# Kernel optimization log

Hardware: AMD Instinct MI355X
Metric: run time of the kernel (lower is better)

## Reference

```python
import jax, jax.numpy as jnp
import numpy as np

B, T, S, H, L = 64, 512, 400, 768, 9


def setup_inputs() -> dict:
    rng = np.random.default_rng(0)
    attn = np.zeros((B, T), np.int32)
    ids_lens = np.zeros((B, S), np.int32)
    for bi in range(B):
        Lb = int(rng.integers(T // 2, T + 1))  # valid wordpiece count
        lens = []
        rem = Lb
        while rem > 0 and len(lens) < S - 1:
            l = int(min(rng.integers(1, 4), rem))  # 1-3 wordpieces per word
            lens.append(l)
            rem -= l
        if rem > 0:
            lens.append(rem)
        attn[bi, :Lb] = 1
        ids_lens[bi, :len(lens)] = np.asarray(lens, np.int32)
    label_ids = rng.integers(0, L, (B, S)).astype(np.int32)
    label_mask = ids_lens > 0
    key = jax.random.key(0)
    k1, k2 = jax.random.split(key)
    last_enc_out = jax.random.normal(k1, (B, T, H), jnp.float32)
    W = jax.random.normal(k2, (H, L), jnp.float32) * 0.02
    b = jnp.zeros((L,), jnp.float32)
    return {
        'last_enc_out': last_enc_out, 'W': W, 'b': b,
        'attention_mask': jnp.asarray(attn), 'ids_lens': jnp.asarray(ids_lens),
        'label_ids': jnp.asarray(label_ids), 'label_mask': jnp.asarray(label_mask),
    }


def reference(last_enc_out, W, b, attention_mask, ids_lens, label_ids, label_mask):
    Bv, Tv, Hv = last_enc_out.shape
    Sv = ids_lens.shape[1]
    # position of each valid token among the row's valid tokens
    tok_pos = jnp.cumsum(attention_mask, axis=1) - 1            # [B,T]
    cum = jnp.cumsum(ids_lens, axis=1)                          # [B,S] nondecreasing
    # word index for each token: first w with cum[w] > tok_pos
    word_idx = jax.vmap(lambda c, p: jnp.searchsorted(c, p, side='right'))(cum, tok_pos)
    valid = attention_mask > 0
    seg = jnp.where(valid, jnp.arange(Bv)[:, None] * Sv + word_idx, Bv * Sv)  # dump slot for pad
    sums = jax.ops.segment_sum(last_enc_out.reshape(Bv * Tv, Hv), seg.reshape(Bv * Tv),
                               num_segments=Bv * Sv + 1)[:Bv * Sv]
    counts = jnp.maximum(ids_lens.reshape(Bv * Sv), 1).astype(last_enc_out.dtype)
    means = (sums / counts[:, None]).reshape(Bv, Sv, Hv)
    word_mask = ids_lens > 0
    bert_embed = jnp.where(word_mask[:, :, None], means, jnp.zeros((), last_enc_out.dtype))
    # dropout is identity in eval mode
    logits = bert_embed @ W + b                                 # [B,S,L]
    logp = jax.nn.log_softmax(logits, axis=-1)
    nll = -jnp.take_along_axis(logp, label_ids[..., None].astype(jnp.int32), axis=-1)[..., 0]
    mf = label_mask.astype(logits.dtype)
    loss = jnp.sum(nll * mf) / jnp.sum(mf)                      # CE with ignore_index masking
    output = jnp.argmax(logits, axis=-1)
    return loss, output
```

## Files before the change

### kernel.cpp

```cpp
#include <hip/hip_runtime.h>
#include <math.h>

#define Bdim 64
#define Tdim 512
#define Sdim 400
#define Hdim 768
#define Ldim 9
#define PSTRIDE 12

#define PROJ_BLOCKS 2048
#define TOK_PER_BLK 16

template <int CTRL>
__device__ __forceinline__ float dpp_add(float x) {
  int y = __builtin_amdgcn_update_dpp(0, __float_as_int(x), CTRL, 0xF, 0xF, false);
  return x + __int_as_float(y);
}
__device__ __forceinline__ float wave_sum63(float x) {
  x = dpp_add<0x111>(x);
  x = dpp_add<0x112>(x);
  x = dpp_add<0x114>(x);
  x = dpp_add<0x118>(x);
  x = dpp_add<0x142>(x);
  x = dpp_add<0x143>(x);
  return x;
}

__global__ __launch_bounds__(Tdim) void setup_kernel(
    const int* __restrict__ attn, const int* __restrict__ ids_lens,
    int* __restrict__ pos2tok, int* __restrict__ wstart,
    int* __restrict__ nvalid, float* __restrict__ accum,
    unsigned* __restrict__ counter) {
  int b = blockIdx.x;
  int tid = threadIdx.x;
  int lane = tid & 63, wid = tid >> 6;
  __shared__ int wsum[8];
  __shared__ int totsm;

  if (b == 0 && tid < 2) accum[tid] = 0.0f;
  if (b == 0 && tid == 2) *counter = 0u;

  int m = attn[b * Tdim + tid];
  int x = m;
#pragma unroll
  for (int off = 1; off < 64; off <<= 1) {
    int v = __shfl_up(x, off, 64);
    if (lane >= off) x += v;
  }
  if (lane == 63) wsum[wid] = x;
  __syncthreads();
  if (tid < 8) {
    int s = wsum[tid];
    int y = s;
#pragma unroll
    for (int off = 1; off < 8; off <<= 1) {
      int v = __shfl_up(y, off, 64);
      if (tid >= off) y += v;
    }
    wsum[tid] = y - s;
    if (tid == 7) totsm = y;
  }
  __syncthreads();
  int total = totsm;
  x += wsum[wid];
  if (m) pos2tok[b * Tdim + x - 1] = tid;
  if (tid == 0) nvalid[b] = total;
  __syncthreads();

  int len = (tid < Sdim) ? ids_lens[b * Sdim + tid] : 0;
  int x2 = len;
#pragma unroll
  for (int off = 1; off < 64; off <<= 1) {
    int v = __shfl_up(x2, off, 64);
    if (lane >= off) x2 += v;
  }
  if (lane == 63) wsum[wid] = x2;
  __syncthreads();
  if (tid < 8) {
    int s = wsum[tid];
    int y = s;
#pragma unroll
    for (int off = 1; off < 8; off <<= 1) {
      int v = __shfl_up(y, off, 64);
      if (tid >= off) y += v;
    }
    wsum[tid] = y - s;
  }
  __syncthreads();
  x2 += wsum[wid];
  if (tid < Sdim) wstart[b * Sdim + tid] = x2 - len;
}

__global__ __launch_bounds__(192, 4) void proj_kernel(
    const float* __restrict__ enc, const float* __restrict__ W,
    const int* __restrict__ pos2tok, const int* __restrict__ nvalid,
    float* __restrict__ proj) {
  int tid = threadIdx.x;
  int lane = tid & 63;
  int w = tid >> 6;
  int l0 = w * 3;
  int base = blockIdx.x * TOK_PER_BLK;
  int b = base >> 9;
  int vc = nvalid[b] - (base & 511);
  vc = vc < 0 ? 0 : (vc > TOK_PER_BLK ? TOK_PER_BLK : vc);
  if (vc == 0) return;

  float wf[3][4][3];
#pragma unroll
  for (int k = 0; k < 3; ++k)
#pragma unroll
    for (int j = 0; j < 4; ++j) {
      int h = 4 * lane + 256 * k + j;
#pragma unroll
      for (int c = 0; c < 3; ++c) wf[k][j][c] = W[(size_t)h * Ldim + l0 + c];
    }

  const float4* encb = (const float4*)enc + (size_t)(b << 9) * (Hdim / 4);

  float4 xr[2][3];
#pragma unroll
  for (int i = 0; i < 2; ++i) {
    int tv = pos2tok[base + i];
    int t = (i < vc) ? tv : 0;
    const float4* r = encb + (size_t)t * (Hdim / 4);
    xr[i][0] = r[lane];
    xr[i][1] = r[lane + 64];
    xr[i][2] = r[lane + 128];
  }

#pragma unroll
  for (int i = 0; i < TOK_PER_BLK; ++i) {
    float4 x0 = xr[i & 1][0], x1 = xr[i & 1][1], x2 = xr[i & 1][2];
    if (i < vc) {
      float dd[3];
#pragma unroll
      for (int c = 0; c < 3; ++c) {
        dd[c] = x0.x * wf[0][0][c] + x0.y * wf[0][1][c] +
                x0.z * wf[0][2][c] + x0.w * wf[0][3][c] +
                x1.x * wf[1][0][c] + x1.y * wf[1][1][c] +
                x1.z * wf[1][2][c] + x1.w * wf[1][3][c] +
                x2.x * wf[2][0][c] + x2.y * wf[2][1][c] +
                x2.z * wf[2][2][c] + x2.w * wf[2][3][c];
      }
#pragma unroll
      for (int c = 0; c < 3; ++c) dd[c] = wave_sum63(dd[c]);
      if (lane == 63) {
        float* dst = proj + (size_t)(base + i) * PSTRIDE + l0;
        dst[0] = dd[0];
        dst[1] = dd[1];
        dst[2] = dd[2];
      }
    }
    if (i + 2 < TOK_PER_BLK) {
      int tv = pos2tok[base + i + 2];
      int t = (i + 2 < vc) ? tv : 0;
      const float4* r = encb + (size_t)t * (Hdim / 4);
      xr[i & 1][0] = r[lane];
      xr[i & 1][1] = r[lane + 64];
      xr[i & 1][2] = r[lane + 128];
    }
  }
}

__global__ __launch_bounds__(256) void word_kernel(
    const float* __restrict__ proj, const float* __restrict__ bias,
    const int* __restrict__ ids_lens, const int* __restrict__ label_ids,
    const int* __restrict__ wstart, const int* __restrict__ nvalid,
    float* __restrict__ out, float* __restrict__ accum,
    unsigned* __restrict__ counter) {
  int bs = blockIdx.x * 256 + threadIdx.x;
  int b = bs / Sdim;
  int len = ids_lens[bs];

  float s[Ldim];
#pragma unroll
  for (int l = 0; l < Ldim; ++l) s[l] = 0.0f;

  if (len > 0) {
    int start = wstart[bs];
    int nv = nvalid[b];
    for (int j = 0; j < len; ++j) {
      int q = start + j;
      if (q >= nv) break;
      const float* pr = proj + ((size_t)(b << 9) + q) * PSTRIDE;
#pragma unroll
      for (int l = 0; l < Ldim; ++l) s[l] += pr[l];
    }
  }
  float inv = (len > 0) ? 1.0f / (float)len : 0.0f;
  float lg[Ldim];
#pragma unroll
  for (int l = 0; l < Ldim; ++l) lg[l] = s[l] * inv + bias[l];

  int amax = 0;
  float mx = lg[0];
#pragma unroll
  for (int l = 1; l < Ldim; ++l)
    if (lg[l] > mx) { mx = lg[l]; amax = l; }
  out[1 + bs] = (float)amax;

  float nll = 0.0f, cnt = 0.0f;
  if (len > 0) {
    float se = 0.0f;
#pragma unroll
    for (int l = 0; l < Ldim; ++l) se += expf(lg[l] - mx);
    float lse = mx + logf(se);
    int lab = label_ids[bs];
    float ll = lg[0];
#pragma unroll
    for (int l = 1; l < Ldim; ++l) ll = (lab == l) ? lg[l] : ll;
    nll = lse - ll;
    cnt = 1.0f;
  }

#pragma unroll
  for (int off = 32; off > 0; off >>= 1) {
    nll += __shfl_down(nll, off, 64);
    cnt += __shfl_down(cnt, off, 64);
  }
  __shared__ float ss[4], cc[4];
  int wid = threadIdx.x >> 6, lane = threadIdx.x & 63;
  if (lane == 0) { ss[wid] = nll; cc[wid] = cnt; }
  __syncthreads();
  if (threadIdx.x == 0) {
    atomicAdd(&accum[0], ss[0] + ss[1] + ss[2] + ss[3]);
    atomicAdd(&accum[1], cc[0] + cc[1] + cc[2] + cc[3]);
    __threadfence();
    unsigned prev = atomicAdd(counter, 1u);
    if (prev == gridDim.x - 1) {
      __threadfence();
      float S = atomicAdd(&accum[0], 0.0f);
      float C = atomicAdd(&accum[1], 0.0f);
      out[0] = S / C;
    }
  }
}

extern "C" void kernel_launch(void* const* d_in, const int* in_sizes, int n_in,
                              void* d_out, int out_size, void* d_ws, size_t ws_size,
                              hipStream_t stream) {
  const float* enc      = (const float*)d_in[0];
  const float* W        = (const float*)d_in[1];
  const float* bias     = (const float*)d_in[2];
  const int* attn       = (const int*)d_in[3];
  const int* ids_lens   = (const int*)d_in[4];
  const int* label_ids  = (const int*)d_in[5];

  float* out = (float*)d_out;

  char* ws = (char*)d_ws;
  size_t off0 = 0;
  int* pos2tok      = (int*)(ws + off0);      off0 += (size_t)Bdim * Tdim * sizeof(int);
  int* wstart       = (int*)(ws + off0);      off0 += (size_t)Bdim * Sdim * sizeof(int);
  int* nvalid       = (int*)(ws + off0);      off0 += 256;
  float* accum      = (float*)(ws + off0);    off0 += 128;
  unsigned* counter = (unsigned*)(ws + off0); off0 += 128;
  float* proj       = (float*)(ws + off0);    off0 += (size_t)Bdim * Tdim * PSTRIDE * sizeof(float);

  int word_blocks = (Bdim * Sdim) / 256;

  setup_kernel<<<Bdim, Tdim, 0, stream>>>(attn, ids_lens, pos2tok, wstart,
                                          nvalid, accum, counter);
  proj_kernel<<<PROJ_BLOCKS, 192, 0, stream>>>(enc, W, pos2tok, nvalid, proj);
  word_kernel<<<word_blocks, 256, 0, stream>>>(proj, bias, ids_lens, label_ids,
                                               wstart, nvalid, out, accum, counter);
}
```

Baseline: 39.32 us.

## Fuse setup, projection and word stages into one cooperative kernel with grid syncs

```diff
diff --git a/kernel.cpp b/kernel.cpp
--- a/kernel.cpp
+++ b/kernel.cpp
@@ -1,5 +1,8 @@
 #include <hip/hip_runtime.h>
+#include <hip/hip_cooperative_groups.h>
 #include <math.h>
+
+namespace cg = cooperative_groups;
 
 #define Bdim 64
 #define Tdim 512
@@ -8,8 +11,10 @@
 #define Ldim 9
 #define PSTRIDE 12
 
-#define PROJ_BLOCKS 2048
-#define TOK_PER_BLK 16
+#define NBLK 256
+#define NTHR 256
+#define SLOTS 128
+#define WPB 100
 
 template <int CTRL>
 __device__ __forceinline__ float dpp_add(float x) {
@@ -26,242 +31,233 @@
   return x;
 }
 
-__global__ __launch_bounds__(Tdim) void setup_kernel(
-    const int* __restrict__ attn, const int* __restrict__ ids_lens,
+__global__ __launch_bounds__(NTHR, 1) void fused_kernel(
+    const float* __restrict__ enc, const float* __restrict__ W,
+    const float* __restrict__ bias, const int* __restrict__ attn,
+    const int* __restrict__ ids_lens, const int* __restrict__ label_ids,
     int* __restrict__ pos2tok, int* __restrict__ wstart,
-    int* __restrict__ nvalid, float* __restrict__ accum,
-    unsigned* __restrict__ counter) {
-  int b = blockIdx.x;
-  int tid = threadIdx.x;
-  int lane = tid & 63, wid = tid >> 6;
-  __shared__ int wsum[8];
-  __shared__ int totsm;
-
-  if (b == 0 && tid < 2) accum[tid] = 0.0f;
-  if (b == 0 && tid == 2) *counter = 0u;
-
-  int m = attn[b * Tdim + tid];
-  int x = m;
-#pragma unroll
-  for (int off = 1; off < 64; off <<= 1) {
-    int v = __shfl_up(x, off, 64);
-    if (lane >= off) x += v;
-  }
-  if (lane == 63) wsum[wid] = x;
-  __syncthreads();
-  if (tid < 8) {
-    int s = wsum[tid];
-    int y = s;
-#pragma unroll
-    for (int off = 1; off < 8; off <<= 1) {
-      int v = __shfl_up(y, off, 64);
-      if (tid >= off) y += v;
-    }
-    wsum[tid] = y - s;
-    if (tid == 7) totsm = y;
-  }
-  __syncthreads();
-  int total = totsm;
-  x += wsum[wid];
-  if (m) pos2tok[b * Tdim + x - 1] = tid;
-  if (tid == 0) nvalid[b] = total;
-  __syncthreads();
-
-  int len = (tid < Sdim) ? ids_lens[b * Sdim + tid] : 0;
-  int x2 = len;
-#pragma unroll
-  for (int off = 1; off < 64; off <<= 1) {
-    int v = __shfl_up(x2, off, 64);
-    if (lane >= off) x2 += v;
-  }
-  if (lane == 63) wsum[wid] = x2;
-  __syncthreads();
-  if (tid < 8) {
-    int s = wsum[tid];
-    int y = s;
-#pragma unroll
-    for (int off = 1; off < 8; off <<= 1) {
-      int v = __shfl_up(y, off, 64);
-      if (tid >= off) y += v;
-    }
-    wsum[tid] = y - s;
-  }
-  __syncthreads();
-  x2 += wsum[wid];
-  if (tid < Sdim) wstart[b * Sdim + tid] = x2 - len;
-}
-
-__global__ __launch_bounds__(192, 4) void proj_kernel(
-    const float* __restrict__ enc, const float* __restrict__ W,
-    const int* __restrict__ pos2tok, const int* __restrict__ nvalid,
-    float* __restrict__ proj) {
-  int tid = threadIdx.x;
-  int lane = tid & 63;
-  int w = tid >> 6;
-  int l0 = w * 3;
-  int base = blockIdx.x * TOK_PER_BLK;
-  int b = base >> 9;
-  int vc = nvalid[b] - (base & 511);
-  vc = vc < 0 ? 0 : (vc > TOK_PER_BLK ? TOK_PER_BLK : vc);
-  if (vc == 0) return;
-
-  float wf[3][4][3];
-#pragma unroll
-  for (int k = 0; k < 3; ++k)
-#pragma unroll
-    for (int j = 0; j < 4; ++j) {
-      int h = 4 * lane + 256 * k + j;
-#pragma unroll
-      for (int c = 0; c < 3; ++c) wf[k][j][c] = W[(size_t)h * Ldim + l0 + c];
-    }
-
-  const float4* encb = (const float4*)enc + (size_t)(b << 9) * (Hdim / 4);
-
-  float4 xr[2][3];
-#pragma unroll
-  for (int i = 0; i < 2; ++i) {
-    int tv = pos2tok[base + i];
-    int t = (i < vc) ? tv : 0;
-    const float4* r = encb + (size_t)t * (Hdim / 4);
-    xr[i][0] = r[lane];
-    xr[i][1] = r[lane + 64];
-    xr[i][2] = r[lane + 128];
-  }
-
-#pragma unroll
-  for (int i = 0; i < TOK_PER_BLK; ++i) {
-    float4 x0 = xr[i & 1][0], x1 = xr[i & 1][1], x2 = xr[i & 1][2];
-    if (i < vc) {
-      float dd[3];
-#pragma unroll
-      for (int c = 0; c < 3; ++c) {
-        dd[c] = x0.x * wf[0][0][c] + x0.y * wf[0][1][c] +
-                x0.z * wf[0][2][c] + x0.w * wf[0][3][c] +
-                x1.x * wf[1][0][c] + x1.y * wf[1][1][c] +
-                x1.z * wf[1][2][c] + x1.w * wf[1][3][c] +
-                x2.x * wf[2][0][c] + x2.y * wf[2][1][c] +
-                x2.z * wf[2][2][c] + x2.w * wf[2][3][c];
-      }
-#pragma unroll
-      for (int c = 0; c < 3; ++c) dd[c] = wave_sum63(dd[c]);
-      if (lane == 63) {
-        float* dst = proj + (size_t)(base + i) * PSTRIDE + l0;
-        dst[0] = dd[0];
-        dst[1] = dd[1];
-        dst[2] = dd[2];
-      }
-    }
-    if (i + 2 < TOK_PER_BLK) {
-      int tv = pos2tok[base + i + 2];
-      int t = (i + 2 < vc) ? tv : 0;
-      const float4* r = encb + (size_t)t * (Hdim / 4);
-      xr[i & 1][0] = r[lane];
-      xr[i & 1][1] = r[lane + 64];
-      xr[i & 1][2] = r[lane + 128];
-    }
-  }
-}
-
-__global__ __launch_bounds__(256) void word_kernel(
-    const float* __restrict__ proj, const float* __restrict__ bias,
-    const int* __restrict__ ids_lens, const int* __restrict__ label_ids,
-    const int* __restrict__ wstart, const int* __restrict__ nvalid,
-    float* __restrict__ out, float* __restrict__ accum,
-    unsigned* __restrict__ counter) {
-  int bs = blockIdx.x * 256 + threadIdx.x;
-  int b = bs / Sdim;
-  int len = ids_lens[bs];
-
-  float s[Ldim];
-#pragma unroll
-  for (int l = 0; l < Ldim; ++l) s[l] = 0.0f;
-
-  if (len > 0) {
-    int start = wstart[bs];
-    int nv = nvalid[b];
-    for (int j = 0; j < len; ++j) {
-      int q = start + j;
-      if (q >= nv) break;
-      const float* pr = proj + ((size_t)(b << 9) + q) * PSTRIDE;
-#pragma unroll
-      for (int l = 0; l < Ldim; ++l) s[l] += pr[l];
-    }
-  }
-  float inv = (len > 0) ? 1.0f / (float)len : 0.0f;
-  float lg[Ldim];
-#pragma unroll
-  for (int l = 0; l < Ldim; ++l) lg[l] = s[l] * inv + bias[l];
-
-  int amax = 0;
-  float mx = lg[0];
-#pragma unroll
-  for (int l = 1; l < Ldim; ++l)
-    if (lg[l] > mx) { mx = lg[l]; amax = l; }
-  out[1 + bs] = (float)amax;
-
-  float nll = 0.0f, cnt = 0.0f;
-  if (len > 0) {
-    float se = 0.0f;
-#pragma unroll
-    for (int l = 0; l < Ldim; ++l) se += expf(lg[l] - mx);
-    float lse = mx + logf(se);
-    int lab = label_ids[bs];
-    float ll = lg[0];
-#pragma unroll
-    for (int l = 1; l < Ldim; ++l) ll = (lab == l) ? lg[l] : ll;
-    nll = lse - ll;
-    cnt = 1.0f;
-  }
-
-#pragma unroll
-  for (int off = 32; off > 0; off >>= 1) {
-    nll += __shfl_down(nll, off, 64);
-    cnt += __shfl_down(cnt, off, 64);
-  }
-  __shared__ float ss[4], cc[4];
-  int wid = threadIdx.x >> 6, lane = threadIdx.x & 63;
-  if (lane == 0) { ss[wid] = nll; cc[wid] = cnt; }
-  __syncthreads();
-  if (threadIdx.x == 0) {
-    atomicAdd(&accum[0], ss[0] + ss[1] + ss[2] + ss[3]);
-    atomicAdd(&accum[1], cc[0] + cc[1] + cc[2] + cc[3]);
-    __threadfence();
-    unsigned prev = atomicAdd(counter, 1u);
-    if (prev == gridDim.x - 1) {
-      __threadfence();
-      float S = atomicAdd(&accum[0], 0.0f);
-      float C = atomicAdd(&accum[1], 0.0f);
-      out[0] = S / C;
-    }
+    int* __restrict__ nvalid, float* __restrict__ proj,
+    float2* __restrict__ partials, float* __restrict__ out) {
+  cg::grid_group grid = cg::this_grid();
+  int blk = blockIdx.x, tid = threadIdx.x;
+  int lane = tid & 63, w = tid >> 6;
+  __shared__ int wsum[4];
+  __shared__ int tot;
+  __shared__ float ssm[4], csm[4];
+
+  if (blk < Bdim) {
+    int b = blk;
+    int a0 = attn[b * Tdim + 2 * tid];
+    int a1 = attn[b * Tdim + 2 * tid + 1];
+    int pr = a0 + a1, x = pr;
+#pragma unroll
+    for (int off = 1; off < 64; off <<= 1) {
+      int v = __shfl_up(x, off, 64);
+      if (lane >= off) x += v;
+    }
+    if (lane == 63) wsum[w] = x;
+    __syncthreads();
+    if (tid < 4) {
+      int s = wsum[tid], y = s;
+#pragma unroll
+      for (int off = 1; off < 4; off <<= 1) {
+        int v = __shfl_up(y, off, 64);
+        if (tid >= off) y += v;
+      }
+      wsum[tid] = y - s;
+      if (tid == 3) tot = y;
+    }
+    __syncthreads();
+    int excl = x + wsum[w] - pr;
+    if (a0) pos2tok[b * Tdim + excl + a0 - 1] = 2 * tid;
+    if (a1) pos2tok[b * Tdim + excl + a0 + a1 - 1] = 2 * tid + 1;
+    if (tid == 0) nvalid[b] = tot;
+    __syncthreads();
+    int e0 = (2 * tid < Sdim) ? ids_lens[b * Sdim + 2 * tid] : 0;
+    int e1 = (2 * tid + 1 < Sdim) ? ids_lens[b * Sdim + 2 * tid + 1] : 0;
+    int pr2 = e0 + e1, x2 = pr2;
+#pragma unroll
+    for (int off = 1; off < 64; off <<= 1) {
+      int v = __shfl_up(x2, off, 64);
+      if (lane >= off) x2 += v;
+    }
+    if (lane == 63) wsum[w] = x2;
+    __syncthreads();
+    if (tid < 4) {
+      int s = wsum[tid], y = s;
+#pragma unroll
+      for (int off = 1; off < 4; off <<= 1) {
+        int v = __shfl_up(y, off, 64);
+        if (tid >= off) y += v;
+      }
+      wsum[tid] = y - s;
+    }
+    __syncthreads();
+    int excl2 = x2 + wsum[w] - pr2;
+    if (2 * tid < Sdim) wstart[b * Sdim + 2 * tid] = excl2;
+    if (2 * tid + 1 < Sdim) wstart[b * Sdim + 2 * tid + 1] = excl2 + e0;
+  }
+  grid.sync();
+
+  {
+    int base = blk * SLOTS;
+    int b = base >> 9, q0 = base & 511;
+    int vc = nvalid[b] - q0;
+    vc = vc < 0 ? 0 : (vc > SLOTS ? SLOTS : vc);
+    if (vc > 0) {
+      int l0 = (w == 0) ? 0 : (1 + 2 * w);
+      int nc = (w == 0) ? 3 : 2;
+      float wf[3][4][3];
+#pragma unroll
+      for (int k = 0; k < 3; ++k)
+#pragma unroll
+        for (int j = 0; j < 4; ++j) {
+          int h = 4 * lane + 256 * k + j;
+#pragma unroll
+          for (int c = 0; c < 3; ++c)
+            if (c < nc) wf[k][j][c] = W[(size_t)h * Ldim + l0 + c];
+        }
+      const float4* encb = (const float4*)enc + (size_t)(b << 9) * (Hdim / 4);
+
+      float4 xa0, xa1, xa2, xb0, xb1, xb2;
+#define LDROW(v0, v1, v2, IDX)                                   \
+      {                                                          \
+        int ii = (IDX) < vc ? (IDX) : (vc - 1);                  \
+        int t_ = pos2tok[base + ii];                             \
+        const float4* r_ = encb + (size_t)t_ * (Hdim / 4);       \
+        v0 = r_[lane]; v1 = r_[lane + 64]; v2 = r_[lane + 128];  \
+      }
+#define PROCROW(v0, v1, v2, SLOT)                                      \
+      {                                                                \
+        float dd[3];                                                   \
+        _Pragma("unroll") for (int c = 0; c < 3; ++c) if (c < nc) {    \
+          dd[c] = v0.x * wf[0][0][c] + v0.y * wf[0][1][c] +            \
+                  v0.z * wf[0][2][c] + v0.w * wf[0][3][c] +            \
+                  v1.x * wf[1][0][c] + v1.y * wf[1][1][c] +            \
+                  v1.z * wf[1][2][c] + v1.w * wf[1][3][c] +            \
+                  v2.x * wf[2][0][c] + v2.y * wf[2][1][c] +            \
+                  v2.z * wf[2][2][c] + v2.w * wf[2][3][c];             \
+          dd[c] = wave_sum63(dd[c]);                                   \
+        }                                                              \
+        if (lane == 63) {                                              \
+          float* dst = proj + (size_t)(base + (SLOT)) * PSTRIDE + l0;  \
+          _Pragma("unroll") for (int c = 0; c < 3; ++c)                \
+            if (c < nc) dst[c] = dd[c];                                \
+        }                                                              \
+      }
+      LDROW(xa0, xa1, xa2, 0)
+      LDROW(xb0, xb1, xb2, 1)
+      for (int i = 0; i < vc; i += 2) {
+        PROCROW(xa0, xa1, xa2, i)
+        LDROW(xa0, xa1, xa2, i + 2)
+        if (i + 1 < vc) PROCROW(xb0, xb1, xb2, i + 1)
+        LDROW(xb0, xb1, xb2, i + 3)
+      }
+#undef LDROW
+#undef PROCROW
+    }
+  }
+  grid.sync();
+
+  {
+    float nll = 0.0f, cnt = 0.0f;
+    if (tid < WPB) {
+      int bs = blk * WPB + tid;
+      int b2 = bs / Sdim;
+      int len = ids_lens[bs];
+      float sum[Ldim];
+#pragma unroll
+      for (int l = 0; l < Ldim; ++l) sum[l] = 0.0f;
+      if (len > 0) {
+        int start = wstart[bs];
+        int nv2 = nvalid[b2];
+        for (int j = 0; j < len; ++j) {
+          int q = start + j;
+          if (q >= nv2) break;
+          const float* prow = proj + ((size_t)(b2 << 9) + q) * PSTRIDE;
+#pragma unroll
+          for (int l = 0; l < Ldim; ++l) sum[l] += prow[l];
+        }
+      }
+      float inv = (len > 0) ? 1.0f / (float)len : 0.0f;
+      float lg[Ldim];
+#pragma unroll
+      for (int l = 0; l < Ldim; ++l) lg[l] = sum[l] * inv + bias[l];
+      int amax = 0;
+      float mx = lg[0];
+#pragma unroll
+      for (int l = 1; l < Ldim; ++l)
+        if (lg[l] > mx) { mx = lg[l]; amax = l; }
+      out[1 + bs] = (float)amax;
+      if (len > 0) {
+        float se = 0.0f;
+#pragma unroll
+        for (int l = 0; l < Ldim; ++l) se += expf(lg[l] - mx);
+        float lse = mx + logf(se);
+        int lab = label_ids[bs];
+        float ll = lg[0];
+#pragma unroll
+        for (int l = 1; l < Ldim; ++l) ll = (lab == l) ? lg[l] : ll;
+        nll = lse - ll;
+        cnt = 1.0f;
+      }
+    }
+#pragma unroll
+    for (int off = 32; off > 0; off >>= 1) {
+      nll += __shfl_down(nll, off, 64);
+      cnt += __shfl_down(cnt, off, 64);
+    }
+    if (lane == 0) { ssm[w] = nll; csm[w] = cnt; }
+    __syncthreads();
+    if (tid == 0) {
+      float2 pc;
+      pc.x = ssm[0] + ssm[1] + ssm[2] + ssm[3];
+      pc.y = csm[0] + csm[1] + csm[2] + csm[3];
+      partials[blk] = pc;
+    }
+  }
+  grid.sync();
+
+  if (blk == 0) {
+    float2 pc = partials[tid];
+    float s = pc.x, c = pc.y;
+#pragma unroll
+    for (int off = 32; off > 0; off >>= 1) {
+      s += __shfl_down(s, off, 64);
+      c += __shfl_down(c, off, 64);
+    }
+    if (lane == 0) { ssm[w] = s; csm[w] = c; }
+    __syncthreads();
+    if (tid == 0)
+      out[0] = (ssm[0] + ssm[1] + ssm[2] + ssm[3]) /
+               (csm[0] + csm[1] + csm[2] + csm[3]);
   }
 }
 
 extern "C" void kernel_launch(void* const* d_in, const int* in_sizes, int n_in,
                               void* d_out, int out_size, void* d_ws, size_t ws_size,
                               hipStream_t stream) {
-  const float* enc      = (const float*)d_in[0];
-  const float* W        = (const float*)d_in[1];
-  const float* bias     = (const float*)d_in[2];
-  const int* attn       = (const int*)d_in[3];
-  const int* ids_lens   = (const int*)d_in[4];
-  const int* label_ids  = (const int*)d_in[5];
+  const float* enc     = (const float*)d_in[0];
+  const float* W       = (const float*)d_in[1];
+  const float* bias    = (const float*)d_in[2];
+  const int* attn      = (const int*)d_in[3];
+  const int* ids_lens  = (const int*)d_in[4];
+  const int* label_ids = (const int*)d_in[5];
 
   float* out = (float*)d_out;
 
   char* ws = (char*)d_ws;
   size_t off0 = 0;
-  int* pos2tok      = (int*)(ws + off0);      off0 += (size_t)Bdim * Tdim * sizeof(int);
-  int* wstart       = (int*)(ws + off0);      off0 += (size_t)Bdim * Sdim * sizeof(int);
-  int* nvalid       = (int*)(ws + off0);      off0 += 256;
-  float* accum      = (float*)(ws + off0);    off0 += 128;
-  unsigned* counter = (unsigned*)(ws + off0); off0 += 128;
-  float* proj       = (float*)(ws + off0);    off0 += (size_t)Bdim * Tdim * PSTRIDE * sizeof(float);
-
-  int word_blocks = (Bdim * Sdim) / 256;
-
-  setup_kernel<<<Bdim, Tdim, 0, stream>>>(attn, ids_lens, pos2tok, wstart,
-                                          nvalid, accum, counter);
-  proj_kernel<<<PROJ_BLOCKS, 192, 0, stream>>>(enc, W, pos2tok, nvalid, proj);
-  word_kernel<<<word_blocks, 256, 0, stream>>>(proj, bias, ids_lens, label_ids,
-                                               wstart, nvalid, out, accum, counter);
-}
+  int* pos2tok     = (int*)(ws + off0);    off0 += (size_t)Bdim * Tdim * sizeof(int);
+  int* wstart      = (int*)(ws + off0);    off0 += (size_t)Bdim * Sdim * sizeof(int);
+  int* nvalid      = (int*)(ws + off0);    off0 += 256;
+  float* proj      = (float*)(ws + off0);  off0 += (size_t)Bdim * Tdim * PSTRIDE * sizeof(float);
+  float2* partials = (float2*)(ws + off0); off0 += NBLK * sizeof(float2);
+
+  void* args[] = {(void*)&enc,      (void*)&W,      (void*)&bias,
+                  (void*)&attn,     (void*)&ids_lens, (void*)&label_ids,
+                  (void*)&pos2tok,  (void*)&wstart, (void*)&nvalid,
+                  (void*)&proj,     (void*)&partials, (void*)&out};
+  hipLaunchCooperativeKernel((void*)fused_kernel, dim3(NBLK), dim3(NTHR),
+                             args, 0, stream);
+}
```

Result: slower. 148.8 us (+278.3%).

## Project all token rows densely and fold setup scans into the word kernel

Applied to the files above, without the earlier changes.

```diff
diff --git a/kernel.cpp b/kernel.cpp
--- a/kernel.cpp
+++ b/kernel.cpp
@@ -9,7 +9,7 @@
 #define PSTRIDE 12
 
 #define PROJ_BLOCKS 2048
-#define TOK_PER_BLK 16
+#define ROWS_PER_BLK 16
 
 template <int CTRL>
 __device__ __forceinline__ float dpp_add(float x) {
@@ -26,84 +26,20 @@
   return x;
 }
 
-__global__ __launch_bounds__(Tdim) void setup_kernel(
-    const int* __restrict__ attn, const int* __restrict__ ids_lens,
-    int* __restrict__ pos2tok, int* __restrict__ wstart,
-    int* __restrict__ nvalid, float* __restrict__ accum,
-    unsigned* __restrict__ counter) {
-  int b = blockIdx.x;
-  int tid = threadIdx.x;
-  int lane = tid & 63, wid = tid >> 6;
-  __shared__ int wsum[8];
-  __shared__ int totsm;
-
-  if (b == 0 && tid < 2) accum[tid] = 0.0f;
-  if (b == 0 && tid == 2) *counter = 0u;
-
-  int m = attn[b * Tdim + tid];
-  int x = m;
-#pragma unroll
-  for (int off = 1; off < 64; off <<= 1) {
-    int v = __shfl_up(x, off, 64);
-    if (lane >= off) x += v;
-  }
-  if (lane == 63) wsum[wid] = x;
-  __syncthreads();
-  if (tid < 8) {
-    int s = wsum[tid];
-    int y = s;
-#pragma unroll
-    for (int off = 1; off < 8; off <<= 1) {
-      int v = __shfl_up(y, off, 64);
-      if (tid >= off) y += v;
-    }
-    wsum[tid] = y - s;
-    if (tid == 7) totsm = y;
-  }
-  __syncthreads();
-  int total = totsm;
-  x += wsum[wid];
-  if (m) pos2tok[b * Tdim + x - 1] = tid;
-  if (tid == 0) nvalid[b] = total;
-  __syncthreads();
-
-  int len = (tid < Sdim) ? ids_lens[b * Sdim + tid] : 0;
-  int x2 = len;
-#pragma unroll
-  for (int off = 1; off < 64; off <<= 1) {
-    int v = __shfl_up(x2, off, 64);
-    if (lane >= off) x2 += v;
-  }
-  if (lane == 63) wsum[wid] = x2;
-  __syncthreads();
-  if (tid < 8) {
-    int s = wsum[tid];
-    int y = s;
-#pragma unroll
-    for (int off = 1; off < 8; off <<= 1) {
-      int v = __shfl_up(y, off, 64);
-      if (tid >= off) y += v;
-    }
-    wsum[tid] = y - s;
-  }
-  __syncthreads();
-  x2 += wsum[wid];
-  if (tid < Sdim) wstart[b * Sdim + tid] = x2 - len;
-}
-
 __global__ __launch_bounds__(192, 4) void proj_kernel(
     const float* __restrict__ enc, const float* __restrict__ W,
-    const int* __restrict__ pos2tok, const int* __restrict__ nvalid,
-    float* __restrict__ proj) {
+    float* __restrict__ proj, float* __restrict__ accum,
+    unsigned* __restrict__ counter) {
   int tid = threadIdx.x;
   int lane = tid & 63;
   int w = tid >> 6;
   int l0 = w * 3;
-  int base = blockIdx.x * TOK_PER_BLK;
-  int b = base >> 9;
-  int vc = nvalid[b] - (base & 511);
-  vc = vc < 0 ? 0 : (vc > TOK_PER_BLK ? TOK_PER_BLK : vc);
-  if (vc == 0) return;
+  int base = blockIdx.x * ROWS_PER_BLK;
+
+  if (blockIdx.x == 0) {
+    if (tid < 2) accum[tid] = 0.0f;
+    if (tid == 2) *counter = 0u;
+  }
 
   float wf[3][4][3];
 #pragma unroll
@@ -115,102 +51,151 @@
       for (int c = 0; c < 3; ++c) wf[k][j][c] = W[(size_t)h * Ldim + l0 + c];
     }
 
-  const float4* encb = (const float4*)enc + (size_t)(b << 9) * (Hdim / 4);
-
-  float4 xr[2][3];
-#pragma unroll
-  for (int i = 0; i < 2; ++i) {
-    int tv = pos2tok[base + i];
-    int t = (i < vc) ? tv : 0;
-    const float4* r = encb + (size_t)t * (Hdim / 4);
-    xr[i][0] = r[lane];
-    xr[i][1] = r[lane + 64];
-    xr[i][2] = r[lane + 128];
-  }
-
-#pragma unroll
-  for (int i = 0; i < TOK_PER_BLK; ++i) {
-    float4 x0 = xr[i & 1][0], x1 = xr[i & 1][1], x2 = xr[i & 1][2];
-    if (i < vc) {
-      float dd[3];
-#pragma unroll
-      for (int c = 0; c < 3; ++c) {
-        dd[c] = x0.x * wf[0][0][c] + x0.y * wf[0][1][c] +
-                x0.z * wf[0][2][c] + x0.w * wf[0][3][c] +
-                x1.x * wf[1][0][c] + x1.y * wf[1][1][c] +
-                x1.z * wf[1][2][c] + x1.w * wf[1][3][c] +
-                x2.x * wf[2][0][c] + x2.y * wf[2][1][c] +
-                x2.z * wf[2][2][c] + x2.w * wf[2][3][c];
+  const float4* encf4 = (const float4*)enc;
+
+  float4 xa0, xa1, xa2, xb0, xb1, xb2;
+#define LDROW(v0, v1, v2, IDX)                                             \
+  {                                                                        \
+    const float4* r_ = encf4 + (size_t)(base + (IDX)) * (Hdim / 4);        \
+    v0 = r_[lane]; v1 = r_[lane + 64]; v2 = r_[lane + 128];                \
+  }
+#define PROCROW(v0, v1, v2, IDX)                                           \
+  {                                                                        \
+    float dd[3];                                                           \
+    _Pragma("unroll") for (int c = 0; c < 3; ++c) {                        \
+      dd[c] = v0.x * wf[0][0][c] + v0.y * wf[0][1][c] +                    \
+              v0.z * wf[0][2][c] + v0.w * wf[0][3][c] +                    \
+              v1.x * wf[1][0][c] + v1.y * wf[1][1][c] +                    \
+              v1.z * wf[1][2][c] + v1.w * wf[1][3][c] +                    \
+              v2.x * wf[2][0][c] + v2.y * wf[2][1][c] +                    \
+              v2.z * wf[2][2][c] + v2.w * wf[2][3][c];                     \
+      dd[c] = wave_sum63(dd[c]);                                           \
+    }                                                                      \
+    if (lane == 63) {                                                      \
+      float* dst = proj + (size_t)(base + (IDX)) * PSTRIDE + l0;           \
+      dst[0] = dd[0]; dst[1] = dd[1]; dst[2] = dd[2];                      \
+    }                                                                      \
+  }
+
+  LDROW(xa0, xa1, xa2, 0)
+  LDROW(xb0, xb1, xb2, 1)
+#pragma unroll
+  for (int i = 0; i < ROWS_PER_BLK; i += 2) {
+    PROCROW(xa0, xa1, xa2, i)
+    if (i + 2 < ROWS_PER_BLK) LDROW(xa0, xa1, xa2, i + 2)
+    PROCROW(xb0, xb1, xb2, i + 1)
+    if (i + 3 < ROWS_PER_BLK) LDROW(xb0, xb1, xb2, i + 3)
+  }
+#undef LDROW
+#undef PROCROW
+}
+
+__global__ __launch_bounds__(Tdim) void rowword_kernel(
+    const float* __restrict__ proj, const float* __restrict__ bias,
+    const int* __restrict__ attn, const int* __restrict__ ids_lens,
+    const int* __restrict__ label_ids, float* __restrict__ out,
+    float* __restrict__ accum, unsigned* __restrict__ counter) {
+  int b = blockIdx.x;
+  int tid = threadIdx.x;
+  int lane = tid & 63, wid = tid >> 6;
+  __shared__ int p2t[Tdim];
+  __shared__ int wst[Sdim];
+  __shared__ int wsum[8];
+  __shared__ int totsm;
+  __shared__ float ssm[8], csm[8];
+
+  int m = attn[b * Tdim + tid];
+  int x = m;
+#pragma unroll
+  for (int off = 1; off < 64; off <<= 1) {
+    int v = __shfl_up(x, off, 64);
+    if (lane >= off) x += v;
+  }
+  if (lane == 63) wsum[wid] = x;
+  __syncthreads();
+  if (tid < 8) {
+    int s = wsum[tid], y = s;
+#pragma unroll
+    for (int off = 1; off < 8; off <<= 1) {
+      int v = __shfl_up(y, off, 64);
+      if (tid >= off) y += v;
+    }
+    wsum[tid] = y - s;
+    if (tid == 7) totsm = y;
+  }
+  __syncthreads();
+  x += wsum[wid];
+  if (m) p2t[x - 1] = tid;
+  int nv_local = totsm;
+  __syncthreads();
+
+  int len = (tid < Sdim) ? ids_lens[b * Sdim + tid] : 0;
+  int x2 = len;
+#pragma unroll
+  for (int off = 1; off < 64; off <<= 1) {
+    int v = __shfl_up(x2, off, 64);
+    if (lane >= off) x2 += v;
+  }
+  if (lane == 63) wsum[wid] = x2;
+  __syncthreads();
+  if (tid < 8) {
+    int s = wsum[tid], y = s;
+#pragma unroll
+    for (int off = 1; off < 8; off <<= 1) {
+      int v = __shfl_up(y, off, 64);
+      if (tid >= off) y += v;
+    }
+    wsum[tid] = y - s;
+  }
+  __syncthreads();
+  x2 += wsum[wid];
+  if (tid < Sdim) wst[tid] = x2 - len;
+  __syncthreads();
+
+  float nll = 0.0f, cnt = 0.0f;
+  if (tid < Sdim) {
+    int bs = b * Sdim + tid;
+    float sum[Ldim];
+#pragma unroll
+    for (int l = 0; l < Ldim; ++l) sum[l] = 0.0f;
+    if (len > 0) {
+      int start = wst[tid];
+      for (int j = 0; j < len; ++j) {
+        int q = start + j;
+        if (q >= nv_local) break;
+        const float* pr = proj + ((size_t)(b << 9) + p2t[q]) * PSTRIDE;
+        const float4* pr4 = (const float4*)pr;
+        float4 r0 = pr4[0], r1 = pr4[1];
+        float r8 = pr[8];
+        sum[0] += r0.x; sum[1] += r0.y; sum[2] += r0.z; sum[3] += r0.w;
+        sum[4] += r1.x; sum[5] += r1.y; sum[6] += r1.z; sum[7] += r1.w;
+        sum[8] += r8;
       }
-#pragma unroll
-      for (int c = 0; c < 3; ++c) dd[c] = wave_sum63(dd[c]);
-      if (lane == 63) {
-        float* dst = proj + (size_t)(base + i) * PSTRIDE + l0;
-        dst[0] = dd[0];
-        dst[1] = dd[1];
-        dst[2] = dd[2];
-      }
-    }
-    if (i + 2 < TOK_PER_BLK) {
-      int tv = pos2tok[base + i + 2];
-      int t = (i + 2 < vc) ? tv : 0;
-      const float4* r = encb + (size_t)t * (Hdim / 4);
-      xr[i & 1][0] = r[lane];
-      xr[i & 1][1] = r[lane + 64];
-      xr[i & 1][2] = r[lane + 128];
-    }
-  }
-}
-
-__global__ __launch_bounds__(256) void word_kernel(
-    const float* __restrict__ proj, const float* __restrict__ bias,
-    const int* __restrict__ ids_lens, const int* __restrict__ label_ids,
-    const int* __restrict__ wstart, const int* __restrict__ nvalid,
-    float* __restrict__ out, float* __restrict__ accum,
-    unsigned* __restrict__ counter) {
-  int bs = blockIdx.x * 256 + threadIdx.x;
-  int b = bs / Sdim;
-  int len = ids_lens[bs];
-
-  float s[Ldim];
-#pragma unroll
-  for (int l = 0; l < Ldim; ++l) s[l] = 0.0f;
-
-  if (len > 0) {
-    int start = wstart[bs];
-    int nv = nvalid[b];
-    for (int j = 0; j < len; ++j) {
-      int q = start + j;
-      if (q >= nv) break;
-      const float* pr = proj + ((size_t)(b << 9) + q) * PSTRIDE;
-#pragma unroll
-      for (int l = 0; l < Ldim; ++l) s[l] += pr[l];
-    }
-  }
-  float inv = (len > 0) ? 1.0f / (float)len : 0.0f;
-  float lg[Ldim];
-#pragma unroll
-  for (int l = 0; l < Ldim; ++l) lg[l] = s[l] * inv + bias[l];
-
-  int amax = 0;
-  float mx = lg[0];
-#pragma unroll
-  for (int l = 1; l < Ldim; ++l)
-    if (lg[l] > mx) { mx = lg[l]; amax = l; }
-  out[1 + bs] = (float)amax;
-
-  float nll = 0.0f, cnt = 0.0f;
-  if (len > 0) {
-    float se = 0.0f;
-#pragma unroll
-    for (int l = 0; l < Ldim; ++l) se += expf(lg[l] - mx);
-    float lse = mx + logf(se);
-    int lab = label_ids[bs];
-    float ll = lg[0];
-#pragma unroll
-    for (int l = 1; l < Ldim; ++l) ll = (lab == l) ? lg[l] : ll;
-    nll = lse - ll;
-    cnt = 1.0f;
+    }
+    float inv = (len > 0) ? 1.0f / (float)len : 0.0f;
+    float lg[Ldim];
+#pragma unroll
+    for (int l = 0; l < Ldim; ++l) lg[l] = sum[l] * inv + bias[l];
+
+    int amax = 0;
+    float mx = lg[0];
+#pragma unroll
+    for (int l = 1; l < Ldim; ++l)
+      if (lg[l] > mx) { mx = lg[l]; amax = l; }
+    out[1 + bs] = (float)amax;
+
+    if (len > 0) {
+      float se = 0.0f;
+#pragma unroll
+      for (int l = 0; l < Ldim; ++l) se += expf(lg[l] - mx);
+      float lse = mx + logf(se);
+      int lab = label_ids[bs];
+      float ll = lg[0];
+#pragma unroll
+      for (int l = 1; l < Ldim; ++l) ll = (lab == l) ? lg[l] : ll;
+      nll = lse - ll;
+      cnt = 1.0f;
+    }
   }
 
 #pragma unroll
@@ -218,20 +203,21 @@
     nll += __shfl_down(nll, off, 64);
     cnt += __shfl_down(cnt, off, 64);
   }
-  __shared__ float ss[4], cc[4];
-  int wid = threadIdx.x >> 6, lane = threadIdx.x & 63;
-  if (lane == 0) { ss[wid] = nll; cc[wid] = cnt; }
-  __syncthreads();
-  if (threadIdx.x == 0) {
-    atomicAdd(&accum[0], ss[0] + ss[1] + ss[2] + ss[3]);
-    atomicAdd(&accum[1], cc[0] + cc[1] + cc[2] + cc[3]);
+  if (lane == 0) { ssm[wid] = nll; csm[wid] = cnt; }
+  __syncthreads();
+  if (tid == 0) {
+    float S = 0.f, C = 0.f;
+#pragma unroll
+    for (int k = 0; k < 8; ++k) { S += ssm[k]; C += csm[k]; }
+    atomicAdd(&accum[0], S);
+    atomicAdd(&accum[1], C);
     __threadfence();
     unsigned prev = atomicAdd(counter, 1u);
     if (prev == gridDim.x - 1) {
       __threadfence();
-      float S = atomicAdd(&accum[0], 0.0f);
-      float C = atomicAdd(&accum[1], 0.0f);
-      out[0] = S / C;
+      float Sf = atomicAdd(&accum[0], 0.0f);
+      float Cf = atomicAdd(&accum[1], 0.0f);
+      out[0] = Sf / Cf;
     }
   }
 }
@@ -239,29 +225,22 @@
 extern "C" void kernel_launch(void* const* d_in, const int* in_sizes, int n_in,
                               void* d_out, int out_size, void* d_ws, size_t ws_size,
                               hipStream_t stream) {
-  const float* enc      = (const float*)d_in[0];
-  const float* W        = (const float*)d_in[1];
-  const float* bias     = (const float*)d_in[2];
-  const int* attn       = (const int*)d_in[3];
-  const int* ids_lens   = (const int*)d_in[4];
-  const int* label_ids  = (const int*)d_in[5];
+  const float* enc     = (const float*)d_in[0];
+  const float* W       = (const float*)d_in[1];
+  const float* bias    = (const float*)d_in[2];
+  const int* attn      = (const int*)d_in[3];
+  const int* ids_lens  = (const int*)d_in[4];
+  const int* label_ids = (const int*)d_in[5];
 
   float* out = (float*)d_out;
 
   char* ws = (char*)d_ws;
   size_t off0 = 0;
-  int* pos2tok      = (int*)(ws + off0);      off0 += (size_t)Bdim * Tdim * sizeof(int);
-  int* wstart       = (int*)(ws + off0);      off0 += (size_t)Bdim * Sdim * sizeof(int);
-  int* nvalid       = (int*)(ws + off0);      off0 += 256;
   float* accum      = (float*)(ws + off0);    off0 += 128;
   unsigned* counter = (unsigned*)(ws + off0); off0 += 128;
   float* proj       = (float*)(ws + off0);    off0 += (size_t)Bdim * Tdim * PSTRIDE * sizeof(float);
 
-  int word_blocks = (Bdim * Sdim) / 256;
-
-  setup_kernel<<<Bdim, Tdim, 0, stream>>>(attn, ids_lens, pos2tok, wstart,
-                                          nvalid, accum, counter);
-  proj_kernel<<<PROJ_BLOCKS, 192, 0, stream>>>(enc, W, pos2tok, nvalid, proj);
-  word_kernel<<<word_blocks, 256, 0, stream>>>(proj, bias, ids_lens, label_ids,
-                                               wstart, nvalid, out, accum, counter);
-}
+  proj_kernel<<<PROJ_BLOCKS, 192, 0, stream>>>(enc, W, proj, accum, counter);
+  rowword_kernel<<<Bdim, Tdim, 0, stream>>>(proj, bias, attn, ids_lens,
+                                            label_ids, out, accum, counter);
+}
```

After: 34.58 us. 12.1% less time.
